# Performance work log

Measured on AMD Instinct MI355X. Metric: run time of the kernel, lower is better.

## Reference

```python
import jax, jax.numpy as jnp
import numpy as np

DIM, K_RANK, L, N_CLASS = 64, 16, 8, 10
H = 1e-3
B = 256
DD = DIM * DIM  # 4096


def _cay(C, D):
    # Cayley transform of B = C @ D^T : I + C (I - 0.5 D^T C)^{-1} D^T
    Id = jnp.eye(C.shape[1], dtype=C.dtype)
    DT = jnp.swapaxes(D, 1, 2)
    inv = jnp.linalg.inv(Id - 0.5 * DT @ C)
    return Id + C @ inv @ DT


def setup_inputs() -> dict:
    key = jax.random.key(0)
    ks = jax.random.split(key, 9)
    u = jax.random.normal(ks[0], (B, DIM, K_RANK), jnp.float32) / np.float32(np.sqrt(DIM))
    vh = jax.random.normal(ks[1], (B, K_RANK, DIM), jnp.float32) / np.float32(np.sqrt(DIM))
    eye_k = jnp.eye(K_RANK, dtype=jnp.float32)
    off = 0.05 * jax.random.normal(ks[2], (B, K_RANK, K_RANK), jnp.float32) * (1.0 - eye_k)
    dvals = jax.random.uniform(ks[3], (B, K_RANK), jnp.float32, 0.5, 1.5)
    s_core = off + dvals[:, :, None] * eye_k  # diag bounded away from 0 (invert_S)
    s_block = jnp.zeros((B, DIM, K_RANK), jnp.float32).at[:, :K_RANK, :K_RANK].set(s_core)
    X = jnp.stack([u.reshape(B, -1), s_block.reshape(B, -1), vh.reshape(B, -1)], axis=1)
    sc = np.float32(1.0 / np.sqrt(DD))
    W0 = sc * jax.random.normal(ks[4], (DD, DD), jnp.float32)
    W = sc * jax.random.normal(ks[5], (L, DD, DD), jnp.float32)
    b = sc * jax.random.normal(ks[6], (L, DD), jnp.float32)
    Wc = sc * jax.random.normal(ks[7], (N_CLASS, DD), jnp.float32)
    bc = sc * jax.random.normal(ks[8], (N_CLASS,), jnp.float32)
    return {"X": X, "W0": W0, "W": W, "b": b, "Wc": Wc, "bc": bc}


def reference(X, W0, W, b, Wc, bc):
    Bn = X.shape[0]
    u = X[:, 0].reshape(Bn, DIM, K_RANK)
    s = X[:, 1].reshape(Bn, DIM, K_RANK)[:, :K_RANK, :K_RANK]
    vh = X[:, 2].reshape(Bn, K_RANK, DIM)
    v = jnp.swapaxes(vh, 1, 2)
    eye_k = jnp.eye(K_RANK, dtype=X.dtype)
    eye_d = jnp.eye(DIM, dtype=X.dtype)
    Xf = (u @ s @ vh).reshape(Bn, DD)
    outs = []
    for i in range(L + 1):  # layer 0 has no bias
        lin = Xf @ W0.T if i == 0 else Xf @ W[i - 1].T + b[i - 1]
        dY = jax.nn.relu(lin).reshape(Bn, DIM, DIM)
        # invert_S: invert only the diagonal of s
        s_inv = (1.0 / jnp.diagonal(s, axis1=1, axis2=2))[:, :, None] * eye_k
        dU = dY @ v @ s_inv
        dV = jnp.swapaxes(dY, 1, 2) @ u @ jnp.swapaxes(s_inv, 1, 2)
        dS = jnp.swapaxes(u, 1, 2) @ dY @ v
        uT = jnp.swapaxes(u, 1, 2)
        F = (eye_d - u @ uT) @ dU
        FT = jnp.swapaxes(F, 1, 2)
        u = _cay(H * (F @ uT), -H * (u @ FT)) @ u
        vT = jnp.swapaxes(v, 1, 2)
        F = (eye_d - v @ vT) @ dV
        FT = jnp.swapaxes(F, 1, 2)
        v = _cay(H * (F @ vT), -H * (v @ FT)) @ v
        s = s + H * dS
        Xf = (u @ s @ jnp.swapaxes(v, 1, 2)).reshape(Bn, DD)
        outs.append(Xf)
    X_transformed = jnp.stack(outs, axis=-1)  # (B, dim*dim, L+1)
    X_classified = Xf @ Wc.T + bc
    X_predicted = jax.nn.softmax(X_classified, axis=1)
    return X_predicted, X_classified, X_transformed
```

## Files before the change

### kernel.cpp

```cpp
#include <hip/hip_runtime.h>
#include <math.h>

typedef unsigned short u16;
typedef unsigned int u32;
using bf16x8 = __attribute__((ext_vector_type(8))) short;
using f32x4  = __attribute__((ext_vector_type(4))) float;

#define DD 4096
#define NB 256
#define SPLIT_K 4
#define PSTRIDE (NB * DD)
#define PLANE (NB * DD)

__device__ __forceinline__ u16 f2bf(float f) {
  unsigned int u = __float_as_uint(f);
  u += 0x7fffu + ((u >> 16) & 1u);
  return (u16)(u >> 16);
}
__device__ __forceinline__ float bf2f(u16 h) {
  return __uint_as_float((u32)h << 16);
}
__device__ __forceinline__ unsigned int pack2bf(float a, float b) {
  return (unsigned int)f2bf(a) | ((unsigned int)f2bf(b) << 16);
}
__device__ __forceinline__ void async_cp16(const u16* g, u16* l) {
  __builtin_amdgcn_global_load_lds(
      (const __attribute__((address_space(1))) unsigned int*)g,
      (__attribute__((address_space(3))) unsigned int*)l, 16, 0, 0);
}

__global__ __launch_bounds__(512, 8) void gemm_kernel(
    const u16* __restrict__ A, const float* __restrict__ W,
    u16* __restrict__ part)
{
  const int nt = blockIdx.x;
  const int mt = blockIdx.y & 1;
  const int kz = blockIdx.y >> 1;
  const int t = threadIdx.x;
  const int w = t >> 6, l = t & 63;

  __shared__ __align__(16) u16 As[128 * 64];
  __shared__ __align__(16) u16 Bs[64 * 64];

  const int colg0 = nt << 6;
  const int m0 = mt << 7;
  const int k0 = kz << 10;

  f32x4 acc[2][2];
#pragma unroll
  for (int mi = 0; mi < 2; ++mi)
#pragma unroll
    for (int nj = 0; nj < 2; ++nj)
      acc[mi][nj] = (f32x4){0.f, 0.f, 0.f, 0.f};

  const int wm = w & 3, wn = w >> 2;
  const int lr = l & 15, lg = l >> 4;
  const int arow_l = (w << 3) + (l >> 3);
  const int acl = l & 7;
  const int bn_l = t >> 3;
  const int bcc = t & 7;

  for (int tt = 0; tt < 16; ++tt) {
    const int kk = k0 + (tt << 6);
    __syncthreads();
#pragma unroll
    for (int r2 = 0; r2 < 2; ++r2) {
      const int row = (r2 << 6) + arow_l;
      const int cs = acl ^ (row & 7);
      async_cp16(A + ((size_t)(m0 + row) << 12) + kk + (cs << 3),
                 &As[(r2 << 12) + (w << 9)]);
    }
    {
      const float* wsrc = W + ((size_t)(colg0 + bn_l) << 12) + kk + (bcc << 3);
      const float4 f0 = *reinterpret_cast<const float4*>(wsrc);
      const float4 f1 = *reinterpret_cast<const float4*>(wsrc + 4);
      uint4 pk;
      pk.x = pack2bf(f0.x, f0.y);
      pk.y = pack2bf(f0.z, f0.w);
      pk.z = pack2bf(f1.x, f1.y);
      pk.w = pack2bf(f1.z, f1.w);
      *reinterpret_cast<uint4*>(&Bs[(bn_l << 6) + ((bcc ^ (bn_l & 7)) << 3)]) = pk;
    }
    __syncthreads();
#pragma unroll
    for (int ks = 0; ks < 2; ++ks) {
      const int cg = (ks << 2) + lg;
      bf16x8 av[2], bv[2];
#pragma unroll
      for (int mi = 0; mi < 2; ++mi) {
        const int fr = (wm << 5) + (mi << 4) + lr;
        av[mi] = *reinterpret_cast<const bf16x8*>(&As[(fr << 6) + ((cg ^ (fr & 7)) << 3)]);
      }
#pragma unroll
      for (int nj = 0; nj < 2; ++nj) {
        const int fc = (wn << 5) + (nj << 4) + lr;
        bv[nj] = *reinterpret_cast<const bf16x8*>(&Bs[(fc << 6) + ((cg ^ (fc & 7)) << 3)]);
      }
#pragma unroll
      for (int mi = 0; mi < 2; ++mi)
#pragma unroll
        for (int nj = 0; nj < 2; ++nj)
          acc[mi][nj] = __builtin_amdgcn_mfma_f32_16x16x32_bf16(
              av[mi], bv[nj], acc[mi][nj], 0, 0, 0);
    }
  }

  u16* pout = part + (size_t)kz * PSTRIDE;
#pragma unroll
  for (int mi = 0; mi < 2; ++mi)
#pragma unroll
    for (int nj = 0; nj < 2; ++nj) {
      const int col = colg0 + (wn << 5) + (nj << 4) + lr;
#pragma unroll
      for (int j = 0; j < 4; ++j) {
        const int row = m0 + (wm << 5) + (mi << 4) + (lg << 2) + j;
        pout[((size_t)row << 12) + col] = f2bf(acc[mi][nj][j]);
      }
    }
}

struct UpdSmem {
  float U[64][17], V[64][17], P[64][17], Q[64][17];
  float S[16][16];
  float sinv[16];
  union {
    struct {
      float dY[64][68];
      float dYT[64][69];
    };
    struct {
      float F[64][17];
      float T1[16][17], G1[16][17], G2[16][17], M1[16][17], dSs[16][17];
      float RS[512];
    };
  };
};

__device__ __forceinline__ void stiefel_update512(
    UpdSmem& m, float (&Am)[64][17], float (&Dm)[64][17],
    int t, float* __restrict__ gout, size_t ub)
{
  const int p = t >> 3;
  const int j0 = (t << 1) & 15;
  {
    const int half = t & 1, i = t >> 5, j = (t >> 1) & 15;
    float a = 0.f;
    const int r0 = half << 5;
    for (int r = r0; r < r0 + 32; ++r) a += Am[r][i] * Dm[r][j];
    m.RS[t] = a;
  }
  __syncthreads();
  if (t < 256) m.T1[t >> 4][t & 15] = m.RS[t << 1] + m.RS[(t << 1) + 1];
  __syncthreads();
  {
    float f0 = Dm[p][j0], f1 = Dm[p][j0 + 1];
    for (int k = 0; k < 16; ++k) {
      const float ak = Am[p][k];
      f0 -= ak * m.T1[k][j0];
      f1 -= ak * m.T1[k][j0 + 1];
    }
    m.F[p][j0] = f0; m.F[p][j0 + 1] = f1;
  }
  __syncthreads();
  if (t < 256) {
    const int i = t >> 4, j = t & 15;
    float g = 0.f;
    for (int r = 0; r < 64; ++r) g += Am[r][i] * m.F[r][j];
    m.G1[i][j] = g;
  } else {
    const int tt = t - 256, i = tt >> 4, j = tt & 15;
    float g = 0.f;
    for (int r = 0; r < 64; ++r) g += Am[r][i] * Am[r][j];
    m.G2[i][j] = g;
  }
  __syncthreads();
  if (t < 256) {
    const int i = t >> 4, j = t & 15;
    float mm = 0.f;
    for (int k = 0; k < 16; ++k) mm += m.G1[i][k] * m.G2[k][j];
    m.M1[i][j] = mm;
  }
  __syncthreads();
  {
    float a0 = 0.f, a1 = 0.f;
    for (int k = 0; k < 16; ++k) {
      const float fk = m.F[p][k];
      a0 += fk * m.M1[k][j0];
      a1 += fk * m.M1[k][j0 + 1];
    }
    const float n0 = Am[p][j0] - 1e-6f * a0;
    const float n1 = Am[p][j0 + 1] - 1e-6f * a1;
    __syncthreads();
    Am[p][j0] = n0; Am[p][j0 + 1] = n1;
    *reinterpret_cast<float2*>(gout + ub + (p << 4) + j0) = make_float2(n0, n1);
  }
  __syncthreads();
}

__device__ __forceinline__ void write_xf_tail(
    UpdSmem& m, int t, int b, float* __restrict__ Xf, u16* __restrict__ Xfb,
    float* __restrict__ outL_plane)
{
  const int p = t >> 3;
  const int j0 = (t << 1) & 15;
  {
    float a0 = 0.f, a1 = 0.f;
    for (int k = 0; k < 16; ++k) {
      const float uk = m.U[p][k];
      a0 += uk * m.S[k][j0];
      a1 += uk * m.S[k][j0 + 1];
    }
    m.P[p][j0] = a0; m.P[p][j0 + 1] = a1;
  }
  __syncthreads();
  {
    const int q0 = (t & 7) << 3;
    float res[8];
#pragma unroll
    for (int e = 0; e < 8; ++e) res[e] = 0.f;
    for (int i = 0; i < 16; ++i) {
      const float pi = m.P[p][i];
#pragma unroll
      for (int e = 0; e < 8; ++e) res[e] += pi * m.V[q0 + e][i];
    }
    const size_t ko = ((size_t)b << 12) + (p << 6) + q0;
    float4* xo = reinterpret_cast<float4*>(Xf + ko);
    const float4 r0 = make_float4(res[0], res[1], res[2], res[3]);
    const float4 r1 = make_float4(res[4], res[5], res[6], res[7]);
    xo[0] = r0; xo[1] = r1;
    uint4 pk;
    pk.x = pack2bf(res[0], res[1]); pk.y = pack2bf(res[2], res[3]);
    pk.z = pack2bf(res[4], res[5]); pk.w = pack2bf(res[6], res[7]);
    *reinterpret_cast<uint4*>(Xfb + ko) = pk;
    if (outL_plane != nullptr) {
      float4* op = reinterpret_cast<float4*>(outL_plane + ko);
      op[0] = r0; op[1] = r1;
    }
  }
}

__global__ __launch_bounds__(512) void update_kernel(
    const u16* __restrict__ part, const float* __restrict__ bias,
    float* __restrict__ u_g, float* __restrict__ v_g, float* __restrict__ s_g,
    float* __restrict__ Xf, u16* __restrict__ Xfb,
    float* __restrict__ outL, int layer)
{
  const int b = blockIdx.x, t = threadIdx.x;
  __shared__ __align__(16) UpdSmem m;
  float* outL_plane = outL + (size_t)layer * PLANE;

  const size_t ub = (size_t)b << 10;
  {
    const float2 u2 = *reinterpret_cast<const float2*>(u_g + ub + (t << 1));
    const float2 v2 = *reinterpret_cast<const float2*>(v_g + ub + (t << 1));
    const int r = t >> 3, c = (t & 7) << 1;
    m.U[r][c] = u2.x; m.U[r][c + 1] = u2.y;
    m.V[r][c] = v2.x; m.V[r][c + 1] = v2.y;
    if (t < 256) m.S[t >> 4][t & 15] = s_g[((size_t)b << 8) + t];
  }
  __syncthreads();
  if (t < 16) m.sinv[t] = 1.0f / m.S[t][t];
  {
    const u16* p0 = part + ((size_t)b << 12) + (t << 3);
    float x[8];
#pragma unroll
    for (int e = 0; e < 8; ++e) x[e] = 0.f;
#pragma unroll
    for (int kzi = 0; kzi < SPLIT_K; ++kzi) {
      const uint4 v = *reinterpret_cast<const uint4*>(p0 + (size_t)kzi * PSTRIDE);
      x[0] += bf2f((u16)(v.x & 0xffff)); x[1] += bf2f((u16)(v.x >> 16));
      x[2] += bf2f((u16)(v.y & 0xffff)); x[3] += bf2f((u16)(v.y >> 16));
      x[4] += bf2f((u16)(v.z & 0xffff)); x[5] += bf2f((u16)(v.z >> 16));
      x[6] += bf2f((u16)(v.w & 0xffff)); x[7] += bf2f((u16)(v.w >> 16));
    }
    if (bias != nullptr) {
      const float4 b0 = *reinterpret_cast<const float4*>(bias + (t << 3));
      const float4 b1 = *reinterpret_cast<const float4*>(bias + (t << 3) + 4);
      x[0] += b0.x; x[1] += b0.y; x[2] += b0.z; x[3] += b0.w;
      x[4] += b1.x; x[5] += b1.y; x[6] += b1.z; x[7] += b1.w;
    }
    const int r = t >> 3, c = (t & 7) << 3;
#pragma unroll
    for (int e = 0; e < 8; ++e) x[e] = fmaxf(x[e], 0.f);
    float4* d0 = reinterpret_cast<float4*>(&m.dY[r][c]);
    d0[0] = make_float4(x[0], x[1], x[2], x[3]);
    d0[1] = make_float4(x[4], x[5], x[6], x[7]);
#pragma unroll
    for (int e = 0; e < 8; ++e) m.dYT[c + e][r] = x[e];
  }
  __syncthreads();
  const int p = t >> 3;
  const int j0 = (t << 1) & 15;
  {
    float a0 = 0.f, a1 = 0.f;
    for (int q = 0; q < 64; ++q) {
      const float d = m.dY[p][q];
      a0 += d * m.V[q][j0];
      a1 += d * m.V[q][j0 + 1];
    }
    float b0 = 0.f, b1 = 0.f;
    for (int r = 0; r < 64; ++r) {
      const float d = m.dYT[p][r];
      b0 += d * m.U[r][j0];
      b1 += d * m.U[r][j0 + 1];
    }
    m.P[p][j0] = a0; m.P[p][j0 + 1] = a1;
    m.Q[p][j0] = b0; m.Q[p][j0 + 1] = b1;
  }
  __syncthreads();
  {
    const int half = t & 1, i = t >> 5, j = (t >> 1) & 15;
    float a = 0.f;
    const int r0 = half << 5;
    for (int r = r0; r < r0 + 32; ++r) a += m.U[r][i] * m.P[r][j];
    m.RS[t] = a;
  }
  __syncthreads();
  if (t < 256) m.dSs[t >> 4][t & 15] = m.RS[t << 1] + m.RS[(t << 1) + 1];
  __syncthreads();
  for (int i = t; i < 1024; i += 512) {
    const int r = i >> 4, c = i & 15;
    const float sc = m.sinv[c];
    m.P[r][c] *= sc;
    m.Q[r][c] *= sc;
  }
  __syncthreads();

  stiefel_update512(m, m.U, m.P, t, u_g, ub);
  stiefel_update512(m, m.V, m.Q, t, v_g, ub);

  if (t < 256) {
    const int i = t >> 4, j = t & 15;
    const float ns = m.S[i][j] + 1e-3f * m.dSs[i][j];
    m.S[i][j] = ns;
    s_g[((size_t)b << 8) + t] = ns;
  }
  __syncthreads();
  write_xf_tail(m, t, b, Xf, Xfb, outL_plane);
}

__global__ __launch_bounds__(512) void init_kernel(
    const float* __restrict__ X, float* __restrict__ u_g, float* __restrict__ v_g,
    float* __restrict__ s_g, float* __restrict__ Xf, u16* __restrict__ Xfb)
{
  const int b = blockIdx.x, t = threadIdx.x;
  __shared__ __align__(16) UpdSmem m;
  const float* xb = X + (size_t)b * 3072;
  const size_t ub = (size_t)b << 10;
  {
    const float2 u2 = *reinterpret_cast<const float2*>(xb + (t << 1));
    const int r = t >> 3, c = (t & 7) << 1;
    m.U[r][c] = u2.x; m.U[r][c + 1] = u2.y;
    *reinterpret_cast<float2*>(u_g + ub + (t << 1)) = u2;
    if (t < 256) {
      const float sv = xb[1024 + t];
      m.S[t >> 4][t & 15] = sv;
      s_g[((size_t)b << 8) + t] = sv;
    }
    const float2 v2 = *reinterpret_cast<const float2*>(xb + 2048 + (t << 1));
    const int g2 = t << 1;
    const int iv = g2 >> 6, q = g2 & 63;
    m.V[q][iv] = v2.x; m.V[q + 1][iv] = v2.y;
    v_g[ub + (size_t)q * 16 + iv] = v2.x;
    v_g[ub + (size_t)(q + 1) * 16 + iv] = v2.y;
  }
  __syncthreads();
  write_xf_tail(m, t, b, Xf, Xfb, nullptr);
}

__global__ __launch_bounds__(256) void pack_kernel(
    const float* __restrict__ outL, float* __restrict__ outT)
{
  const int t = threadIdx.x;
  const int base = blockIdx.x << 8;
  __shared__ float buf[256 * 9];
#pragma unroll
  for (int l = 0; l < 9; ++l)
    buf[t * 9 + l] = outL[(size_t)l * PLANE + base + t];
  __syncthreads();
  const float4* b4 = reinterpret_cast<const float4*>(buf);
  float4* o4 = reinterpret_cast<float4*>(outT + (size_t)base * 9);
  for (int i = t; i < 576; i += 256) o4[i] = b4[i];
}

__global__ __launch_bounds__(256) void classifier_kernel(
    const float* __restrict__ Xf, const float* __restrict__ Wc,
    const float* __restrict__ bc, float* __restrict__ pred, float* __restrict__ cls)
{
  const int b = blockIdx.x, t = threadIdx.x;
  const int lane = t & 63, w = t >> 6;
  __shared__ float red[4][10];
  float acc[10];
#pragma unroll
  for (int c = 0; c < 10; ++c) acc[c] = 0.f;
  const float* xr = Xf + ((size_t)b << 12);
  for (int k = t; k < 4096; k += 256) {
    const float x = xr[k];
#pragma unroll
    for (int c = 0; c < 10; ++c) acc[c] += x * Wc[c * 4096 + k];
  }
#pragma unroll
  for (int c = 0; c < 10; ++c)
    for (int off = 32; off; off >>= 1) acc[c] += __shfl_xor(acc[c], off);
  if (lane == 0)
#pragma unroll
    for (int c = 0; c < 10; ++c) red[w][c] = acc[c];
  __syncthreads();
  if (t == 0) {
    float lg[10], ex[10];
    float m = -1e30f;
#pragma unroll
    for (int c = 0; c < 10; ++c) {
      lg[c] = red[0][c] + red[1][c] + red[2][c] + red[3][c] + bc[c];
      m = fmaxf(m, lg[c]);
    }
    float s = 0.f;
#pragma unroll
    for (int c = 0; c < 10; ++c) { ex[c] = expf(lg[c] - m); s += ex[c]; }
    const float inv = 1.f / s;
#pragma unroll
    for (int c = 0; c < 10; ++c) {
      cls[b * 10 + c] = lg[c];
      pred[b * 10 + c] = ex[c] * inv;
    }
  }
}

extern "C" void kernel_launch(void* const* d_in, const int* in_sizes, int n_in,
                              void* d_out, int out_size, void* d_ws, size_t ws_size,
                              hipStream_t stream) {
  (void)in_sizes; (void)n_in; (void)out_size; (void)ws_size;
  const float* X  = (const float*)d_in[0];
  const float* W0 = (const float*)d_in[1];
  const float* W  = (const float*)d_in[2];
  const float* bb = (const float*)d_in[3];
  const float* Wc = (const float*)d_in[4];
  const float* bc = (const float*)d_in[5];

  float* out_pred  = (float*)d_out;
  float* out_cls   = out_pred + 2560;
  float* out_trans = out_pred + 5120;

  char* ws = (char*)d_ws;
  float* Xf   = (float*)(ws);
  u16*   part = (u16*)  (ws + (4ull << 20));
  float* u_g  = (float*)(ws + (36ull << 20));
  float* v_g  = (float*)(ws + (37ull << 20));
  float* s_g  = (float*)(ws + (38ull << 20));
  u16*   Xfb  = (u16*)  (ws + (39ull << 20));
  float* outL = (float*)(ws + (41ull << 20));

  init_kernel<<<NB, 512, 0, stream>>>(X, u_g, v_g, s_g, Xf, Xfb);
  for (int i = 0; i <= 8; ++i) {
    const float* Wl = (i == 0) ? W0 : W + (size_t)(i - 1) * DD * DD;
    gemm_kernel<<<dim3(64, 2 * SPLIT_K), 512, 0, stream>>>(Xfb, Wl, part);
    update_kernel<<<NB, 512, 0, stream>>>(
        part, (i == 0) ? nullptr : (bb + (size_t)(i - 1) * DD),
        u_g, v_g, s_g, Xf, Xfb, outL, i);
  }
  pack_kernel<<<4096, 256, 0, stream>>>(outL, out_trans);
  classifier_kernel<<<NB, 256, 0, stream>>>(Xf, Wc, bc, out_pred, out_cls);
}
```

Before: 439.2 us.

## Fuse per-layer GEMM and Stiefel update into one kernel with atomic barrier

Merges the split-K GEMM and the per-sample update into a single layer kernel. After its GEMM tile each block bumps a per-row-half atomic counter, and 256 of the 512 blocks spin until all GEMM partials for their half are written, then run the update. The pack and classifier kernels are also merged into one launch. This removes roughly nine kernel launches and their gaps, but relies on all 512 blocks being co-resident, since spinning blocks could otherwise deadlock. It also adds spin-wait overhead and raises shared-memory use through the union.

```diff
diff --git a/kernel.cpp b/kernel.cpp
--- a/kernel.cpp
+++ b/kernel.cpp
@@ -29,96 +29,10 @@
       (__attribute__((address_space(3))) unsigned int*)l, 16, 0, 0);
 }
 
-__global__ __launch_bounds__(512, 8) void gemm_kernel(
-    const u16* __restrict__ A, const float* __restrict__ W,
-    u16* __restrict__ part)
-{
-  const int nt = blockIdx.x;
-  const int mt = blockIdx.y & 1;
-  const int kz = blockIdx.y >> 1;
-  const int t = threadIdx.x;
-  const int w = t >> 6, l = t & 63;
-
-  __shared__ __align__(16) u16 As[128 * 64];
-  __shared__ __align__(16) u16 Bs[64 * 64];
-
-  const int colg0 = nt << 6;
-  const int m0 = mt << 7;
-  const int k0 = kz << 10;
-
-  f32x4 acc[2][2];
-#pragma unroll
-  for (int mi = 0; mi < 2; ++mi)
-#pragma unroll
-    for (int nj = 0; nj < 2; ++nj)
-      acc[mi][nj] = (f32x4){0.f, 0.f, 0.f, 0.f};
-
-  const int wm = w & 3, wn = w >> 2;
-  const int lr = l & 15, lg = l >> 4;
-  const int arow_l = (w << 3) + (l >> 3);
-  const int acl = l & 7;
-  const int bn_l = t >> 3;
-  const int bcc = t & 7;
-
-  for (int tt = 0; tt < 16; ++tt) {
-    const int kk = k0 + (tt << 6);
-    __syncthreads();
-#pragma unroll
-    for (int r2 = 0; r2 < 2; ++r2) {
-      const int row = (r2 << 6) + arow_l;
-      const int cs = acl ^ (row & 7);
-      async_cp16(A + ((size_t)(m0 + row) << 12) + kk + (cs << 3),
-                 &As[(r2 << 12) + (w << 9)]);
-    }
-    {
-      const float* wsrc = W + ((size_t)(colg0 + bn_l) << 12) + kk + (bcc << 3);
-      const float4 f0 = *reinterpret_cast<const float4*>(wsrc);
-      const float4 f1 = *reinterpret_cast<const float4*>(wsrc + 4);
-      uint4 pk;
-      pk.x = pack2bf(f0.x, f0.y);
-      pk.y = pack2bf(f0.z, f0.w);
-      pk.z = pack2bf(f1.x, f1.y);
-      pk.w = pack2bf(f1.z, f1.w);
-      *reinterpret_cast<uint4*>(&Bs[(bn_l << 6) + ((bcc ^ (bn_l & 7)) << 3)]) = pk;
-    }
-    __syncthreads();
-#pragma unroll
-    for (int ks = 0; ks < 2; ++ks) {
-      const int cg = (ks << 2) + lg;
-      bf16x8 av[2], bv[2];
-#pragma unroll
-      for (int mi = 0; mi < 2; ++mi) {
-        const int fr = (wm << 5) + (mi << 4) + lr;
-        av[mi] = *reinterpret_cast<const bf16x8*>(&As[(fr << 6) + ((cg ^ (fr & 7)) << 3)]);
-      }
-#pragma unroll
-      for (int nj = 0; nj < 2; ++nj) {
-        const int fc = (wn << 5) + (nj << 4) + lr;
-        bv[nj] = *reinterpret_cast<const bf16x8*>(&Bs[(fc << 6) + ((cg ^ (fc & 7)) << 3)]);
-      }
-#pragma unroll
-      for (int mi = 0; mi < 2; ++mi)
-#pragma unroll
-        for (int nj = 0; nj < 2; ++nj)
-          acc[mi][nj] = __builtin_amdgcn_mfma_f32_16x16x32_bf16(
-              av[mi], bv[nj], acc[mi][nj], 0, 0, 0);
-    }
-  }
-
-  u16* pout = part + (size_t)kz * PSTRIDE;
-#pragma unroll
-  for (int mi = 0; mi < 2; ++mi)
-#pragma unroll
-    for (int nj = 0; nj < 2; ++nj) {
-      const int col = colg0 + (wn << 5) + (nj << 4) + lr;
-#pragma unroll
-      for (int j = 0; j < 4; ++j) {
-        const int row = m0 + (wm << 5) + (mi << 4) + (lg << 2) + j;
-        pout[((size_t)row << 12) + col] = f2bf(acc[mi][nj][j]);
-      }
-    }
-}
-
+struct GemmSmem {
+  u16 As[128 * 64];
+  u16 Bs[64 * 64];
+};
 struct UpdSmem {
   float U[64][17], V[64][17], P[64][17], Q[64][17];
   float S[16][16];
@@ -135,6 +49,89 @@
     };
   };
 };
+union LayerSmem { GemmSmem g; UpdSmem u; };
+
+__device__ __forceinline__ void gemm_phase(
+    GemmSmem& sm, const u16* __restrict__ A, const float* __restrict__ W,
+    u16* __restrict__ part, int nt, int mt, int kz, int t)
+{
+  const int w = t >> 6, l = t & 63;
+  const int colg0 = nt << 6;
+  const int m0 = mt << 7;
+  const int k0 = kz << 10;
+
+  f32x4 acc[2][2];
+#pragma unroll
+  for (int mi = 0; mi < 2; ++mi)
+#pragma unroll
+    for (int nj = 0; nj < 2; ++nj)
+      acc[mi][nj] = (f32x4){0.f, 0.f, 0.f, 0.f};
+
+  const int wm = w & 3, wn = w >> 2;
+  const int lr = l & 15, lg = l >> 4;
+  const int arow_l = (w << 3) + (l >> 3);
+  const int acl = l & 7;
+  const int bn_l = t >> 3;
+  const int bcc = t & 7;
+
+  for (int tt = 0; tt < 16; ++tt) {
+    const int kk = k0 + (tt << 6);
+    __syncthreads();
+#pragma unroll
+    for (int r2 = 0; r2 < 2; ++r2) {
+      const int row = (r2 << 6) + arow_l;
+      const int cs = acl ^ (row & 7);
+      async_cp16(A + ((size_t)(m0 + row) << 12) + kk + (cs << 3),
+                 &sm.As[(r2 << 12) + (w << 9)]);
+    }
+    {
+      const float* wsrc = W + ((size_t)(colg0 + bn_l) << 12) + kk + (bcc << 3);
+      const float4 f0 = *reinterpret_cast<const float4*>(wsrc);
+      const float4 f1 = *reinterpret_cast<const float4*>(wsrc + 4);
+      uint4 pk;
+      pk.x = pack2bf(f0.x, f0.y);
+      pk.y = pack2bf(f0.z, f0.w);
+      pk.z = pack2bf(f1.x, f1.y);
+      pk.w = pack2bf(f1.z, f1.w);
+      *reinterpret_cast<uint4*>(&sm.Bs[(bn_l << 6) + ((bcc ^ (bn_l & 7)) << 3)]) = pk;
+    }
+    __syncthreads();
+#pragma unroll
+    for (int ks = 0; ks < 2; ++ks) {
+      const int cg = (ks << 2) + lg;
+      bf16x8 av[2], bv[2];
+#pragma unroll
+      for (int mi = 0; mi < 2; ++mi) {
+        const int fr = (wm << 5) + (mi << 4) + lr;
+        av[mi] = *reinterpret_cast<const bf16x8*>(&sm.As[(fr << 6) + ((cg ^ (fr & 7)) << 3)]);
+      }
+#pragma unroll
+      for (int nj = 0; nj < 2; ++nj) {
+        const int fc = (wn << 5) + (nj << 4) + lr;
+        bv[nj] = *reinterpret_cast<const bf16x8*>(&sm.Bs[(fc << 6) + ((cg ^ (fc & 7)) << 3)]);
+      }
+#pragma unroll
+      for (int mi = 0; mi < 2; ++mi)
+#pragma unroll
+        for (int nj = 0; nj < 2; ++nj)
+          acc[mi][nj] = __builtin_amdgcn_mfma_f32_16x16x32_bf16(
+              av[mi], bv[nj], acc[mi][nj], 0, 0, 0);
+    }
+  }
+
+  u16* pout = part + (size_t)kz * PSTRIDE;
+#pragma unroll
+  for (int mi = 0; mi < 2; ++mi)
+#pragma unroll
+    for (int nj = 0; nj < 2; ++nj) {
+      const int col = colg0 + (wn << 5) + (nj << 4) + lr;
+#pragma unroll
+      for (int j = 0; j < 4; ++j) {
+        const int row = m0 + (wm << 5) + (mi << 4) + (lg << 2) + j;
+        pout[((size_t)row << 12) + col] = f2bf(acc[mi][nj][j]);
+      }
+    }
+}
 
 __device__ __forceinline__ void stiefel_update512(
     UpdSmem& m, float (&Am)[64][17], float (&Dm)[64][17],
@@ -239,16 +236,12 @@
   }
 }
 
-__global__ __launch_bounds__(512) void update_kernel(
-    const u16* __restrict__ part, const float* __restrict__ bias,
+__device__ __forceinline__ void update_phase(
+    UpdSmem& m, const u16* __restrict__ part, const float* __restrict__ bias,
     float* __restrict__ u_g, float* __restrict__ v_g, float* __restrict__ s_g,
     float* __restrict__ Xf, u16* __restrict__ Xfb,
-    float* __restrict__ outL, int layer)
-{
-  const int b = blockIdx.x, t = threadIdx.x;
-  __shared__ __align__(16) UpdSmem m;
-  float* outL_plane = outL + (size_t)layer * PLANE;
-
+    float* __restrict__ outL_plane, int b, int t)
+{
   const size_t ub = (size_t)b << 10;
   {
     const float2 u2 = *reinterpret_cast<const float2*>(u_g + ub + (t << 1));
@@ -339,12 +332,48 @@
   write_xf_tail(m, t, b, Xf, Xfb, outL_plane);
 }
 
+__global__ __launch_bounds__(512, 4) void layer_kernel(
+    const u16* __restrict__ A, const float* __restrict__ W,
+    u16* __restrict__ part, const float* __restrict__ bias,
+    float* __restrict__ u_g, float* __restrict__ v_g, float* __restrict__ s_g,
+    float* __restrict__ Xf, u16* __restrict__ Xfb,
+    float* __restrict__ outL_plane, u32* __restrict__ ctr2)
+{
+  __shared__ __align__(16) LayerSmem sm;
+  const int bid = blockIdx.x, t = threadIdx.x;
+  const int nt = bid & 63;
+  const int rest = bid >> 6;
+  const int mt = rest & 1;
+  const int kz = rest >> 1;
+
+  gemm_phase(sm.g, A, W, part, nt, mt, kz, t);
+
+  __syncthreads();
+  if (t == 0) {
+    __threadfence();
+    __hip_atomic_fetch_add(&ctr2[mt], 1u, __ATOMIC_RELEASE,
+                           __HIP_MEMORY_SCOPE_AGENT);
+  }
+  const int idx = (nt << 2) | kz;
+  if (idx >= 128) return;
+  const int b = (mt << 7) | idx;
+  if (t == 0) {
+    while (__hip_atomic_load(&ctr2[mt], __ATOMIC_ACQUIRE,
+                             __HIP_MEMORY_SCOPE_AGENT) < 256u)
+      __builtin_amdgcn_s_sleep(32);
+  }
+  __syncthreads();
+  update_phase(sm.u, part, bias, u_g, v_g, s_g, Xf, Xfb, outL_plane, b, t);
+}
+
 __global__ __launch_bounds__(512) void init_kernel(
     const float* __restrict__ X, float* __restrict__ u_g, float* __restrict__ v_g,
-    float* __restrict__ s_g, float* __restrict__ Xf, u16* __restrict__ Xfb)
+    float* __restrict__ s_g, float* __restrict__ Xf, u16* __restrict__ Xfb,
+    u32* __restrict__ ctrs)
 {
   const int b = blockIdx.x, t = threadIdx.x;
   __shared__ __align__(16) UpdSmem m;
+  if (b == 0 && t < 18) ctrs[t] = 0;
   const float* xb = X + (size_t)b * 3072;
   const size_t ub = (size_t)b << 10;
   {
@@ -368,28 +397,29 @@
   write_xf_tail(m, t, b, Xf, Xfb, nullptr);
 }
 
-__global__ __launch_bounds__(256) void pack_kernel(
-    const float* __restrict__ outL, float* __restrict__ outT)
+__global__ __launch_bounds__(256) void pack_cls_kernel(
+    const float* __restrict__ outL, float* __restrict__ outT,
+    const float* __restrict__ Xf, const float* __restrict__ Wc,
+    const float* __restrict__ bc, float* __restrict__ pred,
+    float* __restrict__ cls)
 {
   const int t = threadIdx.x;
-  const int base = blockIdx.x << 8;
+  const int bid = blockIdx.x;
   __shared__ float buf[256 * 9];
-#pragma unroll
-  for (int l = 0; l < 9; ++l)
-    buf[t * 9 + l] = outL[(size_t)l * PLANE + base + t];
-  __syncthreads();
-  const float4* b4 = reinterpret_cast<const float4*>(buf);
-  float4* o4 = reinterpret_cast<float4*>(outT + (size_t)base * 9);
-  for (int i = t; i < 576; i += 256) o4[i] = b4[i];
-}
-
-__global__ __launch_bounds__(256) void classifier_kernel(
-    const float* __restrict__ Xf, const float* __restrict__ Wc,
-    const float* __restrict__ bc, float* __restrict__ pred, float* __restrict__ cls)
-{
-  const int b = blockIdx.x, t = threadIdx.x;
+  __shared__ float red[4][10];
+  {
+    const int base = bid << 8;
+#pragma unroll
+    for (int l = 0; l < 9; ++l)
+      buf[t * 9 + l] = outL[(size_t)l * PLANE + base + t];
+    __syncthreads();
+    const float4* b4 = reinterpret_cast<const float4*>(buf);
+    float4* o4 = reinterpret_cast<float4*>(outT + (size_t)base * 9);
+    for (int i = t; i < 576; i += 256) o4[i] = b4[i];
+  }
+  if (bid >= NB) return;
+  const int b = bid;
   const int lane = t & 63, w = t >> 6;
-  __shared__ float red[4][10];
   float acc[10];
 #pragma unroll
   for (int c = 0; c < 10; ++c) acc[c] = 0.f;
@@ -408,15 +438,15 @@
   __syncthreads();
   if (t == 0) {
     float lg[10], ex[10];
-    float m = -1e30f;
+    float mx = -1e30f;
 #pragma unroll
     for (int c = 0; c < 10; ++c) {
       lg[c] = red[0][c] + red[1][c] + red[2][c] + red[3][c] + bc[c];
-      m = fmaxf(m, lg[c]);
+      mx = fmaxf(mx, lg[c]);
     }
     float s = 0.f;
 #pragma unroll
-    for (int c = 0; c < 10; ++c) { ex[c] = expf(lg[c] - m); s += ex[c]; }
+    for (int c = 0; c < 10; ++c) { ex[c] = expf(lg[c] - mx); s += ex[c]; }
     const float inv = 1.f / s;
 #pragma unroll
     for (int c = 0; c < 10; ++c) {
@@ -448,16 +478,16 @@
   float* v_g  = (float*)(ws + (37ull << 20));
   float* s_g  = (float*)(ws + (38ull << 20));
   u16*   Xfb  = (u16*)  (ws + (39ull << 20));
+  u32*   ctrs = (u32*)  (ws + (40ull << 20));
   float* outL = (float*)(ws + (41ull << 20));
 
-  init_kernel<<<NB, 512, 0, stream>>>(X, u_g, v_g, s_g, Xf, Xfb);
+  init_kernel<<<NB, 512, 0, stream>>>(X, u_g, v_g, s_g, Xf, Xfb, ctrs);
   for (int i = 0; i <= 8; ++i) {
     const float* Wl = (i == 0) ? W0 : W + (size_t)(i - 1) * DD * DD;
-    gemm_kernel<<<dim3(64, 2 * SPLIT_K), 512, 0, stream>>>(Xfb, Wl, part);
-    update_kernel<<<NB, 512, 0, stream>>>(
-        part, (i == 0) ? nullptr : (bb + (size_t)(i - 1) * DD),
-        u_g, v_g, s_g, Xf, Xfb, outL, i);
-  }
-  pack_kernel<<<4096, 256, 0, stream>>>(outL, out_trans);
-  classifier_kernel<<<NB, 256, 0, stream>>>(Xf, Wc, bc, out_pred, out_cls);
-}
+    layer_kernel<<<512, 512, 0, stream>>>(
+        Xfb, Wl, part, (i == 0) ? nullptr : (bb + (size_t)(i - 1) * DD),
+        u_g, v_g, s_g, Xf, Xfb, outL + (size_t)i * PLANE, ctrs + 2 * i);
+  }
+  pack_cls_kernel<<<4096, 256, 0, stream>>>(outL, out_trans, Xf, Wc, bc,
+                                            out_pred, out_cls);
+}
```

Result: slower. 850.9 us (+93.7%).

## Fuse U and V Stiefel updates and reuse dS as projection term

Applied to the files above, without the earlier changes.

Runs the U and V Stiefel updates together, with half the threads working on each, which removes many block barriers from the per-layer update kernel. The projection term U^T P is computed once and reused as dS, since both equal u^T dY v. The diagonal inverse scaling is applied after the projection instead of in a separate pass. The sinv load now reads straight from global memory before the first barrier. The risk is that each thread now does serial 64-long dot products instead of split halves, and shared memory grows.

```diff
diff --git a/kernel.cpp b/kernel.cpp
--- a/kernel.cpp
+++ b/kernel.cpp
@@ -129,73 +129,14 @@
       float dYT[64][69];
     };
     struct {
-      float F[64][17];
-      float T1[16][17], G1[16][17], G2[16][17], M1[16][17], dSs[16][17];
-      float RS[512];
+      float Fu[64][17], Fv[64][17];
+      float R[16][17], Rv[16][17];
+      float G1u[16][17], G1v[16][17];
+      float G2u[16][17], G2v[16][17];
+      float M1u[16][17], M1v[16][17];
     };
   };
 };
-
-__device__ __forceinline__ void stiefel_update512(
-    UpdSmem& m, float (&Am)[64][17], float (&Dm)[64][17],
-    int t, float* __restrict__ gout, size_t ub)
-{
-  const int p = t >> 3;
-  const int j0 = (t << 1) & 15;
-  {
-    const int half = t & 1, i = t >> 5, j = (t >> 1) & 15;
-    float a = 0.f;
-    const int r0 = half << 5;
-    for (int r = r0; r < r0 + 32; ++r) a += Am[r][i] * Dm[r][j];
-    m.RS[t] = a;
-  }
-  __syncthreads();
-  if (t < 256) m.T1[t >> 4][t & 15] = m.RS[t << 1] + m.RS[(t << 1) + 1];
-  __syncthreads();
-  {
-    float f0 = Dm[p][j0], f1 = Dm[p][j0 + 1];
-    for (int k = 0; k < 16; ++k) {
-      const float ak = Am[p][k];
-      f0 -= ak * m.T1[k][j0];
-      f1 -= ak * m.T1[k][j0 + 1];
-    }
-    m.F[p][j0] = f0; m.F[p][j0 + 1] = f1;
-  }
-  __syncthreads();
-  if (t < 256) {
-    const int i = t >> 4, j = t & 15;
-    float g = 0.f;
-    for (int r = 0; r < 64; ++r) g += Am[r][i] * m.F[r][j];
-    m.G1[i][j] = g;
-  } else {
-    const int tt = t - 256, i = tt >> 4, j = tt & 15;
-    float g = 0.f;
-    for (int r = 0; r < 64; ++r) g += Am[r][i] * Am[r][j];
-    m.G2[i][j] = g;
-  }
-  __syncthreads();
-  if (t < 256) {
-    const int i = t >> 4, j = t & 15;
-    float mm = 0.f;
-    for (int k = 0; k < 16; ++k) mm += m.G1[i][k] * m.G2[k][j];
-    m.M1[i][j] = mm;
-  }
-  __syncthreads();
-  {
-    float a0 = 0.f, a1 = 0.f;
-    for (int k = 0; k < 16; ++k) {
-      const float fk = m.F[p][k];
-      a0 += fk * m.M1[k][j0];
-      a1 += fk * m.M1[k][j0 + 1];
-    }
-    const float n0 = Am[p][j0] - 1e-6f * a0;
-    const float n1 = Am[p][j0 + 1] - 1e-6f * a1;
-    __syncthreads();
-    Am[p][j0] = n0; Am[p][j0 + 1] = n1;
-    *reinterpret_cast<float2*>(gout + ub + (p << 4) + j0) = make_float2(n0, n1);
-  }
-  __syncthreads();
-}
 
 __device__ __forceinline__ void write_xf_tail(
     UpdSmem& m, int t, int b, float* __restrict__ Xf, u16* __restrict__ Xfb,
@@ -248,8 +189,10 @@
   const int b = blockIdx.x, t = threadIdx.x;
   __shared__ __align__(16) UpdSmem m;
   float* outL_plane = outL + (size_t)layer * PLANE;
-
   const size_t ub = (size_t)b << 10;
+  const int p = t >> 3;
+  const int j0 = (t << 1) & 15;
+
   {
     const float2 u2 = *reinterpret_cast<const float2*>(u_g + ub + (t << 1));
     const float2 v2 = *reinterpret_cast<const float2*>(v_g + ub + (t << 1));
@@ -257,10 +200,7 @@
     m.U[r][c] = u2.x; m.U[r][c + 1] = u2.y;
     m.V[r][c] = v2.x; m.V[r][c + 1] = v2.y;
     if (t < 256) m.S[t >> 4][t & 15] = s_g[((size_t)b << 8) + t];
-  }
-  __syncthreads();
-  if (t < 16) m.sinv[t] = 1.0f / m.S[t][t];
-  {
+    if (t < 16)  m.sinv[t] = 1.0f / s_g[((size_t)b << 8) + t * 17];
     const u16* p0 = part + ((size_t)b << 12) + (t << 3);
     float x[8];
 #pragma unroll
@@ -279,18 +219,17 @@
       x[0] += b0.x; x[1] += b0.y; x[2] += b0.z; x[3] += b0.w;
       x[4] += b1.x; x[5] += b1.y; x[6] += b1.z; x[7] += b1.w;
     }
-    const int r = t >> 3, c = (t & 7) << 3;
+    const int r2 = t >> 3, c2 = (t & 7) << 3;
 #pragma unroll
     for (int e = 0; e < 8; ++e) x[e] = fmaxf(x[e], 0.f);
-    float4* d0 = reinterpret_cast<float4*>(&m.dY[r][c]);
+    float4* d0 = reinterpret_cast<float4*>(&m.dY[r2][c2]);
     d0[0] = make_float4(x[0], x[1], x[2], x[3]);
     d0[1] = make_float4(x[4], x[5], x[6], x[7]);
 #pragma unroll
-    for (int e = 0; e < 8; ++e) m.dYT[c + e][r] = x[e];
-  }
-  __syncthreads();
-  const int p = t >> 3;
-  const int j0 = (t << 1) & 15;
+    for (int e = 0; e < 8; ++e) m.dYT[c2 + e][r2] = x[e];
+  }
+  __syncthreads();
+
   {
     float a0 = 0.f, a1 = 0.f;
     for (int q = 0; q < 64; ++q) {
@@ -308,34 +247,104 @@
     m.Q[p][j0] = b0; m.Q[p][j0 + 1] = b1;
   }
   __syncthreads();
-  {
-    const int half = t & 1, i = t >> 5, j = (t >> 1) & 15;
-    float a = 0.f;
-    const int r0 = half << 5;
-    for (int r = r0; r < r0 + 32; ++r) a += m.U[r][i] * m.P[r][j];
-    m.RS[t] = a;
-  }
-  __syncthreads();
-  if (t < 256) m.dSs[t >> 4][t & 15] = m.RS[t << 1] + m.RS[(t << 1) + 1];
-  __syncthreads();
-  for (int i = t; i < 1024; i += 512) {
-    const int r = i >> 4, c = i & 15;
-    const float sc = m.sinv[c];
-    m.P[r][c] *= sc;
-    m.Q[r][c] *= sc;
-  }
-  __syncthreads();
-
-  stiefel_update512(m, m.U, m.P, t, u_g, ub);
-  stiefel_update512(m, m.V, m.Q, t, v_g, ub);
-
-  if (t < 256) {
-    const int i = t >> 4, j = t & 15;
-    const float ns = m.S[i][j] + 1e-3f * m.dSs[i][j];
-    m.S[i][j] = ns;
-    s_g[((size_t)b << 8) + t] = ns;
-  }
-  __syncthreads();
+
+  {
+    const int i = (t >> 4) & 15, j = t & 15;
+    if (t < 256) {
+      float r0 = 0.f, g0 = 0.f;
+      for (int r = 0; r < 64; ++r) {
+        const float ui = m.U[r][i];
+        r0 += ui * m.P[r][j];
+        g0 += ui * m.U[r][j];
+      }
+      m.R[i][j] = r0; m.G2u[i][j] = g0;
+    } else {
+      float r0 = 0.f, g0 = 0.f;
+      for (int r = 0; r < 64; ++r) {
+        const float vi = m.V[r][i];
+        r0 += vi * m.Q[r][j];
+        g0 += vi * m.V[r][j];
+      }
+      m.Rv[i][j] = r0; m.G2v[i][j] = g0;
+    }
+  }
+  __syncthreads();
+
+  {
+    float f0 = m.P[p][j0], f1 = m.P[p][j0 + 1];
+    float g0 = m.Q[p][j0], g1 = m.Q[p][j0 + 1];
+    for (int k = 0; k < 16; ++k) {
+      const float uk = m.U[p][k], vk = m.V[p][k];
+      f0 -= uk * m.R[k][j0];
+      f1 -= uk * m.R[k][j0 + 1];
+      g0 -= vk * m.Rv[k][j0];
+      g1 -= vk * m.Rv[k][j0 + 1];
+    }
+    const float s0 = m.sinv[j0], s1 = m.sinv[j0 + 1];
+    m.Fu[p][j0] = f0 * s0; m.Fu[p][j0 + 1] = f1 * s1;
+    m.Fv[p][j0] = g0 * s0; m.Fv[p][j0 + 1] = g1 * s1;
+  }
+  __syncthreads();
+
+  {
+    const int i = (t >> 4) & 15, j = t & 15;
+    if (t < 256) {
+      float g = 0.f;
+      for (int r = 0; r < 64; ++r) g += m.U[r][i] * m.Fu[r][j];
+      m.G1u[i][j] = g;
+    } else {
+      float g = 0.f;
+      for (int r = 0; r < 64; ++r) g += m.V[r][i] * m.Fv[r][j];
+      m.G1v[i][j] = g;
+    }
+  }
+  __syncthreads();
+
+  {
+    const int i = (t >> 4) & 15, j = t & 15;
+    if (t < 256) {
+      float mm = 0.f;
+      for (int k = 0; k < 16; ++k) mm += m.G1u[i][k] * m.G2u[k][j];
+      m.M1u[i][j] = mm;
+    } else {
+      float mm = 0.f;
+      for (int k = 0; k < 16; ++k) mm += m.G1v[i][k] * m.G2v[k][j];
+      m.M1v[i][j] = mm;
+    }
+  }
+  __syncthreads();
+
+  {
+    float du0 = 0.f, du1 = 0.f, dv0 = 0.f, dv1 = 0.f;
+    for (int k = 0; k < 16; ++k) {
+      const float fu = m.Fu[p][k], fv = m.Fv[p][k];
+      du0 += fu * m.M1u[k][j0];
+      du1 += fu * m.M1u[k][j0 + 1];
+      dv0 += fv * m.M1v[k][j0];
+      dv1 += fv * m.M1v[k][j0 + 1];
+    }
+    const float nu0 = m.U[p][j0]     - 1e-6f * du0;
+    const float nu1 = m.U[p][j0 + 1] - 1e-6f * du1;
+    const float nv0 = m.V[p][j0]     - 1e-6f * dv0;
+    const float nv1 = m.V[p][j0 + 1] - 1e-6f * dv1;
+    float ns = 0.f;
+    if (t < 256) {
+      const int i = t >> 4, j = t & 15;
+      ns = m.S[i][j] + 1e-3f * m.R[i][j];
+    }
+    __syncthreads();
+    m.U[p][j0] = nu0; m.U[p][j0 + 1] = nu1;
+    m.V[p][j0] = nv0; m.V[p][j0 + 1] = nv1;
+    *reinterpret_cast<float2*>(u_g + ub + (p << 4) + j0) = make_float2(nu0, nu1);
+    *reinterpret_cast<float2*>(v_g + ub + (p << 4) + j0) = make_float2(nv0, nv1);
+    if (t < 256) {
+      const int i = t >> 4, j = t & 15;
+      m.S[i][j] = ns;
+      s_g[((size_t)b << 8) + t] = ns;
+    }
+  }
+  __syncthreads();
+
   write_xf_tail(m, t, b, Xf, Xfb, outL_plane);
 }
 
```

New measurement: 420.1 us. -4.4%, faster.
